# Performance work log

Measured on AMD Instinct MI355X. Metric: run time of the kernel, lower is better.

## Reference

```python
import jax, jax.numpy as jnp
import numpy as np

DIM = 768
NUM_HEADS = 12
HEAD_DIM = DIM // NUM_HEADS  # 64
IMG_W = 32
IMG_H = 32
B = 16
N = IMG_W * IMG_H + 1  # 1025 (CLS + grid)


def setup_inputs() -> dict:
    key = jax.random.key(0)
    k1, k2, k3, k4, k5 = jax.random.split(key, 5)
    x = jax.random.normal(k1, (B, N, DIM), dtype=jnp.float32)
    W_qkv = jax.random.normal(k2, (3 * DIM, DIM), dtype=jnp.float32) * 0.02
    W_proj = jax.random.normal(k3, (DIM, DIM), dtype=jnp.float32) * 0.02
    b_proj = jax.random.normal(k4, (DIM,), dtype=jnp.float32) * 0.02
    # learned mixed-RoPE frequencies, shape (2, num_heads * head_dim//2)
    freqs = jax.random.normal(k5, (2, NUM_HEADS * (HEAD_DIM // 2)), dtype=jnp.float32) * 0.1
    return {"x": x, "W_qkv": W_qkv, "W_proj": W_proj, "b_proj": b_proj, "freqs": freqs}


def _mixed_angles(freqs):
    # t_x = t % W, t_y = t // W over the flattened grid (init_t_xy)
    t = jnp.arange(IMG_W * IMG_H, dtype=jnp.float32)
    t_x = t % IMG_W
    t_y = jnp.floor(t / IMG_W)
    # outer products -> (N-1, H, hd/2) -> (H, N-1, hd/2); angle = fx + fy
    fx = (t_x[:, None] * freqs[0][None, :]).reshape(-1, NUM_HEADS, HEAD_DIM // 2)
    fy = (t_y[:, None] * freqs[1][None, :]).reshape(-1, NUM_HEADS, HEAD_DIM // 2)
    return (fx + fy).transpose(1, 0, 2)  # (H, N-1, hd/2)


def _apply_rope(t, cos, sin):
    # t: (B, H, N-1, hd); complex multiply on (even, odd) pairs
    pairs = t.reshape(*t.shape[:-1], HEAD_DIM // 2, 2)
    x0, x1 = pairs[..., 0], pairs[..., 1]
    o0 = x0 * cos - x1 * sin
    o1 = x0 * sin + x1 * cos
    return jnp.stack([o0, o1], axis=-1).reshape(t.shape)


def reference(x, W_qkv, W_proj, b_proj, freqs):
    Bx, Nx, C = x.shape
    scale = HEAD_DIM ** -0.5
    qkv = jnp.einsum('bnc,dc->bnd', x, W_qkv)  # Linear, no bias
    qkv = qkv.reshape(Bx, Nx, 3, NUM_HEADS, HEAD_DIM).transpose(2, 0, 3, 1, 4)
    q, k, v = qkv[0], qkv[1], qkv[2]  # (B, H, N, hd)

    ang = _mixed_angles(freqs)  # (H, N-1, hd/2)
    cos, sin = jnp.cos(ang), jnp.sin(ang)  # broadcast over batch

    # rotate all tokens except the leading CLS token
    q = jnp.concatenate([q[:, :, :1], _apply_rope(q[:, :, 1:], cos, sin)], axis=2)
    k = jnp.concatenate([k[:, :, :1], _apply_rope(k[:, :, 1:], cos, sin)], axis=2)

    attn = jax.nn.softmax(jnp.einsum('bhqd,bhkd->bhqk', q * scale, k), axis=-1)
    out = jnp.einsum('bhqk,bhkd->bhqd', attn, v)  # (B, H, N, hd)
    out = out.transpose(0, 2, 1, 3).reshape(Bx, Nx, C)
    return out @ W_proj.T + b_proj
```

## Files before the change

kernel.cpp:

```cpp
#include <hip/hip_runtime.h>
#include <math.h>

#define DIM     768
#define NH      12
#define HD      64
#define NTOK    1025
#define BATCH   16
#define MTOT    (BATCH * NTOK)
#define QKVD    (3 * DIM)

typedef short  short8  __attribute__((ext_vector_type(8)));
typedef short  short4v __attribute__((ext_vector_type(4)));
typedef float  f32x4   __attribute__((ext_vector_type(4)));

typedef const __attribute__((address_space(1))) void gvoid_t;
typedef __attribute__((address_space(3)))       void lvoid_t;
typedef __attribute__((address_space(3)))       char lchar_t;
#define GLD16(gsrc, ldst) __builtin_amdgcn_global_load_lds( \
    (gvoid_t*)(gsrc), (lvoid_t*)(ldst), 16, 0, 0)

static __device__ __forceinline__ unsigned int f2bf(float f) {
    unsigned int u = __float_as_uint(f);
    u += 0x7FFFu + ((u >> 16) & 1u);
    return u >> 16;
}

__device__ __forceinline__ void cvt8(const float* __restrict__ src,
                                     unsigned short* __restrict__ dst, int i) {
    float4 a = *(const float4*)(src + (size_t)i*8);
    float4 b = *(const float4*)(src + (size_t)i*8 + 4);
    uint4 pk;
    pk.x = f2bf(a.x) | (f2bf(a.y) << 16);
    pk.y = f2bf(a.z) | (f2bf(a.w) << 16);
    pk.z = f2bf(b.x) | (f2bf(b.y) << 16);
    pk.w = f2bf(b.z) | (f2bf(b.w) << 16);
    *(uint4*)(dst + (size_t)i*8) = pk;
}

__global__ __launch_bounds__(256) void cvt_bf16_kernel(
    const float* __restrict__ x, const float* __restrict__ Wq,
    const float* __restrict__ Wp,
    unsigned short* __restrict__ xb, unsigned short* __restrict__ Wqb,
    unsigned short* __restrict__ Wpb)
{
    const int stride = gridDim.x * blockDim.x;
    const int tid = blockIdx.x * blockDim.x + threadIdx.x;
    for (int i = tid; i < MTOT*DIM/8;  i += stride) cvt8(x,  xb,  i);
    for (int i = tid; i < QKVD*DIM/8;  i += stride) cvt8(Wq, Wqb, i);
    for (int i = tid; i < DIM*DIM/8;   i += stride) cvt8(Wp, Wpb, i);
}

__global__ __launch_bounds__(256) void rope_tab_kernel(
    const float* __restrict__ freqs, float2* __restrict__ tab)
{
    const int gid = blockIdx.x * 256 + threadIdx.x;
    const int p  = gid & 31;
    const int n1 = (gid >> 5) & 1023;
    const int h  = gid >> 15;
    const float tx = (float)(n1 & 31), ty = (float)(n1 >> 5);
    const float ang = tx * freqs[h*32 + p] + ty * freqs[384 + h*32 + p];
    float s, c;
    sincosf(ang, &s, &c);
    tab[gid] = make_float2(c, s);
}

__device__ __forceinline__ void gemm_core(
    const unsigned short* __restrict__ Wb,
    const unsigned short* __restrict__ Xb,
    int D0, int T0, int maxXrow,
    short* Ws, short* Xs, f32x4 acc[4][4], int tid)
{
    const int lane = tid & 63;
    const int wu   = __builtin_amdgcn_readfirstlane(tid >> 6);
    const int wr   = wu >> 1, wc = wu & 1;
    const int l4   = lane >> 4, l15 = lane & 15;

    const int srow = lane >> 3;
    const int schk = (lane & 7) ^ srow;
    const unsigned short* wsrc[4];
    const unsigned short* xsrc[4];
#pragma unroll
    for (int i = 0; i < 4; ++i) {
        int r = wu*32 + i*8 + srow;
        wsrc[i] = Wb + (size_t)(D0 + r) * DIM + schk*8;
        int xr = T0 + r; if (xr > maxXrow) xr = maxXrow;
        xsrc[i] = Xb + (size_t)xr * DIM + schk*8;
    }

    for (int kt = 0; kt < DIM/64; ++kt) {
        __syncthreads();
#pragma unroll
        for (int i = 0; i < 4; ++i) {
            GLD16(wsrc[i] + kt*64, &Ws[(wu*4 + i) * 512]);
            GLD16(xsrc[i] + kt*64, &Xs[(wu*4 + i) * 512]);
        }
        __syncthreads();

        short8 wf[4][2], xf[4][2];
#pragma unroll
        for (int f = 0; f < 4; ++f) {
            const int rw = wr*64 + f*16 + l15;
            const int rx = wc*64 + f*16 + l15;
#pragma unroll
            for (int kf = 0; kf < 2; ++kf) {
                wf[f][kf] = *(const short8*)&Ws[rw*64 + (((kf*4 + l4) ^ (rw & 7)) << 3)];
                xf[f][kf] = *(const short8*)&Xs[rx*64 + (((kf*4 + l4) ^ (rx & 7)) << 3)];
            }
        }
        __builtin_amdgcn_s_setprio(1);
#pragma unroll
        for (int kf = 0; kf < 2; ++kf)
#pragma unroll
            for (int fm = 0; fm < 4; ++fm)
#pragma unroll
                for (int fn = 0; fn < 4; ++fn)
                    acc[fm][fn] = __builtin_amdgcn_mfma_f32_16x16x32_bf16(
                        wf[fm][kf], xf[fn][kf], acc[fm][fn], 0, 0, 0);
        __builtin_amdgcn_s_setprio(0);
    }
}

__global__ __launch_bounds__(256) void qkv_gemm_kernel(
    const unsigned short* __restrict__ Wqb, const unsigned short* __restrict__ xb,
    const float2* __restrict__ tab,
    unsigned short* __restrict__ Qb, unsigned short* __restrict__ Kb,
    unsigned short* __restrict__ Vb)
{
    __shared__ __align__(16) short Ws[128*64];
    __shared__ __align__(16) short Xs[128*64];
    f32x4 acc[4][4] = {};
    const int tid = threadIdx.x;

    const int dd0 = blockIdx.x;
    int xc, j;
    if (dd0 >= 2304) { xc = 0; j = 288 + (dd0 - 2304); }
    else             { xc = dd0 & 7; j = dd0 >> 3; }
    const int D0 = (j % 18) * 128;
    const int T0 = (xc + 8 * (j / 18)) * 128;

    gemm_core(Wqb, xb, D0, T0, MTOT - 1, Ws, Xs, acc, tid);

    const int lane = tid & 63;
    const int wu = tid >> 6, wr = wu >> 1, wc = wu & 1;
    const int l4 = lane >> 4, l15 = lane & 15;
    const int which = D0 / DIM;
    unsigned short* dst = (which == 0) ? Qb : (which == 1) ? Kb : Vb;
    const float qs = (which == 0) ? 0.125f * 1.44269504089f : 1.f;

    unsigned bArr[4], nArr[4];
    bool vArr[4];
#pragma unroll
    for (int fn = 0; fn < 4; ++fn) {
        unsigned m = T0 + wc*64 + fn*16 + l15;
        vArr[fn] = m < MTOT;
        bArr[fn] = m / NTOK;
        nArr[fn] = m - bArr[fn]*NTOK;
    }
#pragma unroll
    for (int fm = 0; fm < 4; ++fm) {
        const int hcol = (D0 % DIM) + wr*64 + fm*16 + l4*4;
        const int h = hcol >> 6, dd = hcol & 63;
        const int p0 = dd >> 1;
#pragma unroll
        for (int fn = 0; fn < 4; ++fn) {
            if (!vArr[fn]) continue;
            f32x4 a = acc[fm][fn];
            const int n = nArr[fn];
            if (which < 2) {
                int n1 = n > 0 ? n - 1 : 0;
                float4 cs = *(const float4*)&tab[(size_t)(h*1024 + n1)*32 + p0];
                if (n == 0) cs = make_float4(1.f, 0.f, 1.f, 0.f);
                float e0 = a[0], od0 = a[1], e1 = a[2], od1 = a[3];
                a[0] = e0*cs.x - od0*cs.y;  a[1] = e0*cs.y + od0*cs.x;
                a[2] = e1*cs.z - od1*cs.w;  a[3] = e1*cs.w + od1*cs.z;
            }
            uint2 pk;
            pk.x = f2bf(a[0]*qs) | (f2bf(a[1]*qs) << 16);
            pk.y = f2bf(a[2]*qs) | (f2bf(a[3]*qs) << 16);
            *(uint2*)&dst[((size_t)(bArr[fn]*NH + h)*NTOK + n)*HD + dd] = pk;
        }
    }
}

__global__ __launch_bounds__(256) void attn_mfma_kernel(
    const unsigned short* __restrict__ Qb,
    const unsigned short* __restrict__ Kb,
    const unsigned short* __restrict__ Vb,
    unsigned short* __restrict__ Obf)
{
    __shared__ __align__(16) char KsR[2][8192];
    __shared__ __align__(16) char VtR[2][8192];
    __shared__ __align__(16) char PsR[4][4096];

    const int tid  = threadIdx.x;
    const int lane = tid & 63;
    const int w    = __builtin_amdgcn_readfirstlane(tid >> 6);
    const int l4   = lane >> 4, l15 = lane & 15, l7 = lane & 7;

    const int d    = blockIdx.x;
    const int xcd  = d & 7;
    const int s    = d >> 3;
    const int bh   = xcd * 24 + s / 9;
    const int q0   = (s % 9) * 128;
    const size_t base = (size_t)bh * NTOK * HD;

    short8 qf[2][2];
#pragma unroll
    for (int qg = 0; qg < 2; ++qg) {
        int qr = q0 + w*32 + qg*16 + l15;
        int qrc = qr < NTOK ? qr : NTOK - 1;
        qf[qg][0] = *(const short8*)(Qb + base + (size_t)qrc*HD + l4*8);
        qf[qg][1] = *(const short8*)(Qb + base + (size_t)qrc*HD + 32 + l4*8);
    }

    const short ONE = (short)0x3F80;
    const short8 ones = {ONE, ONE, ONE, ONE, ONE, ONE, ONE, ONE};

    f32x4 oA[4] = {}, oB[4] = {};
    f32x4 laccA = {}, laccB = {};

    const int ktokb = tid >> 3;
    const int kchk  = tid & 7;
    const int c0 = tid, c1 = tid + 256;
    const int vt0 = ((c0 >> 5) << 2) | ((c0 >> 1) & 3);
    const int vt1 = ((c1 >> 5) << 2) | ((c1 >> 1) & 3);
    const int vo0 = (((c0 >> 3) & 3) << 4) | ((c0 & 1) << 3);
    const int vo1 = (((c1 >> 3) & 3) << 4) | ((c1 & 1) << 3);
    char* Pw = &PsR[w][0];

#pragma unroll
    for (int i = 0; i < 2; ++i) {
        int tok = ktokb + i*32;
        int sc = kchk ^ (tok & 7);
        GLD16(Kb + base + (size_t)tok*HD + sc*8, &KsR[0][w*1024 + i*4096]);
    }
    GLD16(Vb + base + (size_t)vt0*HD + vo0, &VtR[0][w*1024]);
    GLD16(Vb + base + (size_t)vt1*HD + vo1, &VtR[0][4096 + w*1024]);

    for (int kt = 0; kt < 17; ++kt) {
        const int buf = kt & 1;
        __syncthreads();

        if (kt < 16) {
            const int nb = buf ^ 1;
#pragma unroll
            for (int i = 0; i < 2; ++i) {
                int tok = ktokb + i*32;
                int gk = (kt+1)*64 + tok; if (gk > NTOK-1) gk = NTOK-1;
                int sc = kchk ^ (tok & 7);
                GLD16(Kb + base + (size_t)gk*HD + sc*8, &KsR[nb][w*1024 + i*4096]);
            }
            int g0 = (kt+1)*64 + vt0; if (g0 > NTOK-1) g0 = NTOK-1;
            int g1 = (kt+1)*64 + vt1; if (g1 > NTOK-1) g1 = NTOK-1;
            GLD16(Vb + base + (size_t)g0*HD + vo0, &VtR[nb][w*1024]);
            GLD16(Vb + base + (size_t)g1*HD + vo1, &VtR[nb][4096 + w*1024]);
        }

        f32x4 sA[4] = {}, sB[4] = {};
        __builtin_amdgcn_s_setprio(1);
#pragma unroll
        for (int tg = 0; tg < 4; ++tg) {
            const int row = tg*16 + l15;
            short8 ka0 = *(const short8*)(&KsR[buf][0] + row*128 + ((l4 ^ l7) << 4));
            short8 ka1 = *(const short8*)(&KsR[buf][0] + row*128 + (((4 + l4) ^ l7) << 4));
            sA[tg] = __builtin_amdgcn_mfma_f32_16x16x32_bf16(ka0, qf[0][0], sA[tg], 0,0,0);
            sA[tg] = __builtin_amdgcn_mfma_f32_16x16x32_bf16(ka1, qf[0][1], sA[tg], 0,0,0);
            sB[tg] = __builtin_amdgcn_mfma_f32_16x16x32_bf16(ka0, qf[1][0], sB[tg], 0,0,0);
            sB[tg] = __builtin_amdgcn_mfma_f32_16x16x32_bf16(ka1, qf[1][1], sB[tg], 0,0,0);
        }
        __builtin_amdgcn_s_setprio(0);

        float pA[16], pB[16];
        if (kt == 16) {
#pragma unroll
            for (int tg = 0; tg < 4; ++tg)
#pragma unroll
                for (int r = 0; r < 4; ++r) {
                    int tok = 1024 + tg*16 + l4*4 + r;
                    float sa = (tok > 1024) ? -3e38f : sA[tg][r];
                    float sb = (tok > 1024) ? -3e38f : sB[tg][r];
                    pA[tg*4+r] = __builtin_exp2f(sa);
                    pB[tg*4+r] = __builtin_exp2f(sb);
                }
        } else {
#pragma unroll
            for (int tg = 0; tg < 4; ++tg)
#pragma unroll
                for (int r = 0; r < 4; ++r) {
                    pA[tg*4+r] = __builtin_exp2f(sA[tg][r]);
                    pB[tg*4+r] = __builtin_exp2f(sB[tg][r]);
                }
        }

#pragma unroll
        for (int tg = 0; tg < 4; ++tg) {
            unsigned k0a, k1a, k0b, k1b;
            asm volatile("v_cvt_pk_bf16_f32 %0, %1, %2" : "=v"(k0a) : "v"(pA[tg*4+0]), "v"(pA[tg*4+1]));
            asm volatile("v_cvt_pk_bf16_f32 %0, %1, %2" : "=v"(k1a) : "v"(pA[tg*4+2]), "v"(pA[tg*4+3]));
            asm volatile("v_cvt_pk_bf16_f32 %0, %1, %2" : "=v"(k0b) : "v"(pB[tg*4+0]), "v"(pB[tg*4+1]));
            asm volatile("v_cvt_pk_bf16_f32 %0, %1, %2" : "=v"(k1b) : "v"(pB[tg*4+2]), "v"(pB[tg*4+3]));
            const int chk = (((tg*2 + (l4 >> 1)) ^ l7) << 4) + (l4 & 1)*8;
            *(uint2*)(Pw + l15*128      + chk) = make_uint2(k0a, k1a);
            *(uint2*)(Pw + (16+l15)*128 + chk) = make_uint2(k0b, k1b);
        }
        __builtin_amdgcn_wave_barrier();

        const short8 pf00 = *(const short8*)(Pw + l15*128      + ((l4 ^ l7) << 4));
        const short8 pf01 = *(const short8*)(Pw + l15*128      + (((4+l4) ^ l7) << 4));
        const short8 pf10 = *(const short8*)(Pw + (16+l15)*128 + ((l4 ^ l7) << 4));
        const short8 pf11 = *(const short8*)(Pw + (16+l15)*128 + (((4+l4) ^ l7) << 4));

        __builtin_amdgcn_s_setprio(1);
        laccA = __builtin_amdgcn_mfma_f32_16x16x32_bf16(ones, pf00, laccA, 0,0,0);
        laccA = __builtin_amdgcn_mfma_f32_16x16x32_bf16(ones, pf01, laccA, 0,0,0);
        laccB = __builtin_amdgcn_mfma_f32_16x16x32_bf16(ones, pf10, laccB, 0,0,0);
        laccB = __builtin_amdgcn_mfma_f32_16x16x32_bf16(ones, pf11, laccB, 0,0,0);
        __builtin_amdgcn_s_setprio(0);

        const unsigned trb = (unsigned)(unsigned long long)
            (lchar_t*)(&VtR[buf][0] + (l4 << 10) + (l15 << 3));
        short4v r0a, r0b, r1a, r1b, r2a, r2b, r3a, r3b;

        asm volatile(
            "ds_read_b64_tr_b16 %0, %8 offset:0\n\t"
            "ds_read_b64_tr_b16 %1, %8 offset:512\n\t"
            "ds_read_b64_tr_b16 %2, %8 offset:128\n\t"
            "ds_read_b64_tr_b16 %3, %8 offset:640\n\t"
            "ds_read_b64_tr_b16 %4, %8 offset:256\n\t"
            "ds_read_b64_tr_b16 %5, %8 offset:768\n\t"
            "ds_read_b64_tr_b16 %6, %8 offset:384\n\t"
            "ds_read_b64_tr_b16 %7, %8 offset:896\n\t"
            "s_waitcnt lgkmcnt(0)"
            : "=&v"(r0a), "=&v"(r0b), "=&v"(r1a), "=&v"(r1b),
              "=&v"(r2a), "=&v"(r2b), "=&v"(r3a), "=&v"(r3b)
            : "v"(trb) : "memory");
        __builtin_amdgcn_sched_barrier(0);
        {
            short8 v0 = __builtin_shufflevector(r0a, r0b, 0,1,2,3,4,5,6,7);
            short8 v1 = __builtin_shufflevector(r1a, r1b, 0,1,2,3,4,5,6,7);
            short8 v2 = __builtin_shufflevector(r2a, r2b, 0,1,2,3,4,5,6,7);
            short8 v3 = __builtin_shufflevector(r3a, r3b, 0,1,2,3,4,5,6,7);
            __builtin_amdgcn_s_setprio(1);
            oA[0] = __builtin_amdgcn_mfma_f32_16x16x32_bf16(v0, pf00, oA[0], 0,0,0);
            oB[0] = __builtin_amdgcn_mfma_f32_16x16x32_bf16(v0, pf10, oB[0], 0,0,0);
            oA[1] = __builtin_amdgcn_mfma_f32_16x16x32_bf16(v1, pf00, oA[1], 0,0,0);
            oB[1] = __builtin_amdgcn_mfma_f32_16x16x32_bf16(v1, pf10, oB[1], 0,0,0);
            oA[2] = __builtin_amdgcn_mfma_f32_16x16x32_bf16(v2, pf00, oA[2], 0,0,0);
            oB[2] = __builtin_amdgcn_mfma_f32_16x16x32_bf16(v2, pf10, oB[2], 0,0,0);
            oA[3] = __builtin_amdgcn_mfma_f32_16x16x32_bf16(v3, pf00, oA[3], 0,0,0);
            oB[3] = __builtin_amdgcn_mfma_f32_16x16x32_bf16(v3, pf10, oB[3], 0,0,0);
            __builtin_amdgcn_s_setprio(0);
        }
        asm volatile(
            "ds_read_b64_tr_b16 %0, %8 offset:4096\n\t"
            "ds_read_b64_tr_b16 %1, %8 offset:4608\n\t"
            "ds_read_b64_tr_b16 %2, %8 offset:4224\n\t"
            "ds_read_b64_tr_b16 %3, %8 offset:4736\n\t"
            "ds_read_b64_tr_b16 %4, %8 offset:4352\n\t"
            "ds_read_b64_tr_b16 %5, %8 offset:4864\n\t"
            "ds_read_b64_tr_b16 %6, %8 offset:4480\n\t"
            "ds_read_b64_tr_b16 %7, %8 offset:4992\n\t"
            "s_waitcnt lgkmcnt(0)"
            : "=&v"(r0a), "=&v"(r0b), "=&v"(r1a), "=&v"(r1b),
              "=&v"(r2a), "=&v"(r2b), "=&v"(r3a), "=&v"(r3b)
            : "v"(trb) : "memory");
        __builtin_amdgcn_sched_barrier(0);
        {
            short8 v0 = __builtin_shufflevector(r0a, r0b, 0,1,2,3,4,5,6,7);
            short8 v1 = __builtin_shufflevector(r1a, r1b, 0,1,2,3,4,5,6,7);
            short8 v2 = __builtin_shufflevector(r2a, r2b, 0,1,2,3,4,5,6,7);
            short8 v3 = __builtin_shufflevector(r3a, r3b, 0,1,2,3,4,5,6,7);
            __builtin_amdgcn_s_setprio(1);
            oA[0] = __builtin_amdgcn_mfma_f32_16x16x32_bf16(v0, pf01, oA[0], 0,0,0);
            oB[0] = __builtin_amdgcn_mfma_f32_16x16x32_bf16(v0, pf11, oB[0], 0,0,0);
            oA[1] = __builtin_amdgcn_mfma_f32_16x16x32_bf16(v1, pf01, oA[1], 0,0,0);
            oB[1] = __builtin_amdgcn_mfma_f32_16x16x32_bf16(v1, pf11, oB[1], 0,0,0);
            oA[2] = __builtin_amdgcn_mfma_f32_16x16x32_bf16(v2, pf01, oA[2], 0,0,0);
            oB[2] = __builtin_amdgcn_mfma_f32_16x16x32_bf16(v2, pf11, oB[2], 0,0,0);
            oA[3] = __builtin_amdgcn_mfma_f32_16x16x32_bf16(v3, pf01, oA[3], 0,0,0);
            oB[3] = __builtin_amdgcn_mfma_f32_16x16x32_bf16(v3, pf11, oB[3], 0,0,0);
            __builtin_amdgcn_s_setprio(0);
        }
    }

    const float liA = 1.f / laccA[0];
    const float liB = 1.f / laccB[0];
    const int b = bh / NH, h = bh % NH;
    const int qA = q0 + w*32 + l15;
    const int qB = qA + 16;
    if (qA < NTOK) {
        unsigned short* p = Obf + ((size_t)b*NTOK + qA)*DIM + h*HD + l4*4;
#pragma unroll
        for (int dg = 0; dg < 4; ++dg) {
            uint2 pk;
            pk.x = f2bf(oA[dg][0]*liA) | (f2bf(oA[dg][1]*liA) << 16);
            pk.y = f2bf(oA[dg][2]*liA) | (f2bf(oA[dg][3]*liA) << 16);
            *(uint2*)(p + dg*16) = pk;
        }
    }
    if (qB < NTOK) {
        unsigned short* p = Obf + ((size_t)b*NTOK + qB)*DIM + h*HD + l4*4;
#pragma unroll
        for (int dg = 0; dg < 4; ++dg) {
            uint2 pk;
            pk.x = f2bf(oB[dg][0]*liB) | (f2bf(oB[dg][1]*liB) << 16);
            pk.y = f2bf(oB[dg][2]*liB) | (f2bf(oB[dg][3]*liB) << 16);
            *(uint2*)(p + dg*16) = pk;
        }
    }
}

__global__ __launch_bounds__(256) void proj_gemm_kernel(
    const unsigned short* __restrict__ Wpb, const unsigned short* __restrict__ Obf,
    const float* __restrict__ bp, float* __restrict__ out)
{
    __shared__ __align__(16) short Ws[128*64];
    __shared__ __align__(16) short Xs[128*64];
    f32x4 acc[4][4] = {};
    const int tid = threadIdx.x;

    const int dd0 = blockIdx.x;
    int xc, j;
    if (dd0 >= 768) { xc = 0; j = 96 + (dd0 - 768); }
    else            { xc = dd0 & 7; j = dd0 >> 3; }
    const int D0 = (j % 6) * 128;
    const int T0 = (xc + 8 * (j / 6)) * 128;

    gemm_core(Wpb, Obf, D0, T0, MTOT - 1, Ws, Xs, acc, tid);

    const int lane = tid & 63;
    const int wu = tid >> 6, wr = wu >> 1, wc = wu & 1;
    const int l4 = lane >> 4, l15 = lane & 15;

    unsigned mArr[4];
    bool vArr[4];
#pragma unroll
    for (int fn = 0; fn < 4; ++fn) {
        unsigned m = T0 + wc*64 + fn*16 + l15;
        mArr[fn] = m;
        vArr[fn] = m < MTOT;
    }
#pragma unroll
    for (int fm = 0; fm < 4; ++fm) {
        const int nG = D0 + wr*64 + fm*16 + l4*4;
        const float4 bias = *(const float4*)&bp[nG];
#pragma unroll
        for (int fn = 0; fn < 4; ++fn) {
            if (!vArr[fn]) continue;
            f32x4 a = acc[fm][fn];
            float4 v = make_float4(a[0]+bias.x, a[1]+bias.y, a[2]+bias.z, a[3]+bias.w);
            *(float4*)&out[(size_t)mArr[fn]*DIM + nG] = v;
        }
    }
}

extern "C" void kernel_launch(void* const* d_in, const int* in_sizes, int n_in,
                              void* d_out, int out_size, void* d_ws, size_t ws_size,
                              hipStream_t stream)
{
    const float* x     = (const float*)d_in[0];
    const float* Wqkv  = (const float*)d_in[1];
    const float* Wp    = (const float*)d_in[2];
    const float* bp    = (const float*)d_in[3];
    const float* freqs = (const float*)d_in[4];
    float* out = (float*)d_out;

    const size_t SZ = (size_t)BATCH * NH * NTOK * HD;
    unsigned short* Qb  = (unsigned short*)d_ws;
    unsigned short* Kb  = Qb + SZ;
    unsigned short* Vb  = Kb + SZ;
    unsigned short* Obf = Vb + SZ;
    unsigned short* xb  = Obf + SZ;
    unsigned short* Wqb = xb + SZ;
    unsigned short* Wpb = Wqb + (size_t)QKVD * DIM;
    float2*         tab = (float2*)(Wpb + (size_t)DIM * DIM);

    cvt_bf16_kernel<<<2048, 256, 0, stream>>>(x, Wqkv, Wp, xb, Wqb, Wpb);
    rope_tab_kernel<<<1536, 256, 0, stream>>>(freqs, tab);
    qkv_gemm_kernel<<<2322, 256, 0, stream>>>(Wqb, xb, tab, Qb, Kb, Vb);
    attn_mfma_kernel<<<1728, 256, 0, stream>>>(Qb, Kb, Vb, Obf);
    proj_gemm_kernel<<<774, 256, 0, stream>>>(Wpb, Obf, bp, out);
}
```

Measured before the change: 263.1 us.

## Switch attention to 32x32x16 MFMA with register-resident P via permlane swaps

The attention kernel moves from 16x16x32 to 32x32x16 bf16 MFMA tiles, with each wave owning 32 query rows as the B operand. The softmax probabilities are converted to bf16 and rearranged in registers with v_permlane32_swap, which removes the per-wave LDS staging buffer, its wave barrier and the reads back. The row sum is now accumulated in scalar float adds plus one cross-half shuffle instead of extra ones-vector MFMAs. The intent is to cut LDS traffic and MFMA issue count, at the cost of larger accumulator register use and trickier lane mappings.

```diff
diff --git a/kernel.cpp b/kernel.cpp
--- a/kernel.cpp
+++ b/kernel.cpp
@@ -12,6 +12,7 @@
 typedef short  short8  __attribute__((ext_vector_type(8)));
 typedef short  short4v __attribute__((ext_vector_type(4)));
 typedef float  f32x4   __attribute__((ext_vector_type(4)));
+typedef float  f32x16  __attribute__((ext_vector_type(16)));
 
 typedef const __attribute__((address_space(1))) void gvoid_t;
 typedef __attribute__((address_space(3)))       void lvoid_t;
@@ -190,34 +191,31 @@
 {
     __shared__ __align__(16) char KsR[2][8192];
     __shared__ __align__(16) char VtR[2][8192];
-    __shared__ __align__(16) char PsR[4][4096];
 
     const int tid  = threadIdx.x;
     const int lane = tid & 63;
     const int w    = __builtin_amdgcn_readfirstlane(tid >> 6);
-    const int l4   = lane >> 4, l15 = lane & 15, l7 = lane & 7;
-
-    const int d    = blockIdx.x;
-    const int xcd  = d & 7;
-    const int s    = d >> 3;
+    const int l31  = lane & 31;
+    const int hh   = lane >> 5;
+
+    const int bid  = blockIdx.x;
+    const int xcd  = bid & 7;
+    const int s    = bid >> 3;
     const int bh   = xcd * 24 + s / 9;
     const int q0   = (s % 9) * 128;
     const size_t base = (size_t)bh * NTOK * HD;
 
-    short8 qf[2][2];
-#pragma unroll
-    for (int qg = 0; qg < 2; ++qg) {
-        int qr = q0 + w*32 + qg*16 + l15;
-        int qrc = qr < NTOK ? qr : NTOK - 1;
-        qf[qg][0] = *(const short8*)(Qb + base + (size_t)qrc*HD + l4*8);
-        qf[qg][1] = *(const short8*)(Qb + base + (size_t)qrc*HD + 32 + l4*8);
-    }
-
-    const short ONE = (short)0x3F80;
-    const short8 ones = {ONE, ONE, ONE, ONE, ONE, ONE, ONE, ONE};
-
-    f32x4 oA[4] = {}, oB[4] = {};
-    f32x4 laccA = {}, laccB = {};
+    const int q  = q0 + w*32 + l31;
+    const int qc = q < NTOK ? q : NTOK - 1;
+    const unsigned short* qp = Qb + base + (size_t)qc*HD + hh*8;
+    const short8 qf0 = *(const short8*)(qp);
+    const short8 qf1 = *(const short8*)(qp + 16);
+    const short8 qf2 = *(const short8*)(qp + 32);
+    const short8 qf3 = *(const short8*)(qp + 48);
+
+    f32x16 o0 = {0,0,0,0,0,0,0,0,0,0,0,0,0,0,0,0};
+    f32x16 o1 = o0;
+    float lsum = 0.f;
 
     const int ktokb = tid >> 3;
     const int kchk  = tid & 7;
@@ -226,7 +224,9 @@
     const int vt1 = ((c1 >> 5) << 2) | ((c1 >> 1) & 3);
     const int vo0 = (((c0 >> 3) & 3) << 4) | ((c0 & 1) << 3);
     const int vo1 = (((c1 >> 3) & 3) << 4) | ((c1 & 1) << 3);
-    char* Pw = &PsR[w][0];
+
+    const unsigned trlane = (unsigned)((hh << 10) | (((lane >> 4) & 1) << 7)
+                                       | ((lane & 15) << 3));
 
 #pragma unroll
     for (int i = 0; i < 2; ++i) {
@@ -256,156 +256,93 @@
             GLD16(Vb + base + (size_t)g1*HD + vo1, &VtR[nb][4096 + w*1024]);
         }
 
-        f32x4 sA[4] = {}, sB[4] = {};
+        const char* Kc = &KsR[buf][0];
+        f32x16 s0 = {0,0,0,0,0,0,0,0,0,0,0,0,0,0,0,0};
+        f32x16 s1 = s0;
         __builtin_amdgcn_s_setprio(1);
 #pragma unroll
-        for (int tg = 0; tg < 4; ++tg) {
-            const int row = tg*16 + l15;
-            short8 ka0 = *(const short8*)(&KsR[buf][0] + row*128 + ((l4 ^ l7) << 4));
-            short8 ka1 = *(const short8*)(&KsR[buf][0] + row*128 + (((4 + l4) ^ l7) << 4));
-            sA[tg] = __builtin_amdgcn_mfma_f32_16x16x32_bf16(ka0, qf[0][0], sA[tg], 0,0,0);
-            sA[tg] = __builtin_amdgcn_mfma_f32_16x16x32_bf16(ka1, qf[0][1], sA[tg], 0,0,0);
-            sB[tg] = __builtin_amdgcn_mfma_f32_16x16x32_bf16(ka0, qf[1][0], sB[tg], 0,0,0);
-            sB[tg] = __builtin_amdgcn_mfma_f32_16x16x32_bf16(ka1, qf[1][1], sB[tg], 0,0,0);
+        for (int g = 0; g < 4; ++g) {
+            const int a = l31*128 + ((((g << 1) | hh) ^ (l31 & 7)) << 4);
+            short8 ka0 = *(const short8*)(Kc + a);
+            short8 ka1 = *(const short8*)(Kc + a + 4096);
+            const short8 qg = (g == 0) ? qf0 : (g == 1) ? qf1 : (g == 2) ? qf2 : qf3;
+            s0 = __builtin_amdgcn_mfma_f32_32x32x16_bf16(ka0, qg, s0, 0, 0, 0);
+            s1 = __builtin_amdgcn_mfma_f32_32x32x16_bf16(ka1, qg, s1, 0, 0, 0);
         }
         __builtin_amdgcn_s_setprio(0);
 
-        float pA[16], pB[16];
         if (kt == 16) {
 #pragma unroll
-            for (int tg = 0; tg < 4; ++tg)
-#pragma unroll
-                for (int r = 0; r < 4; ++r) {
-                    int tok = 1024 + tg*16 + l4*4 + r;
-                    float sa = (tok > 1024) ? -3e38f : sA[tg][r];
-                    float sb = (tok > 1024) ? -3e38f : sB[tg][r];
-                    pA[tg*4+r] = __builtin_exp2f(sa);
-                    pB[tg*4+r] = __builtin_exp2f(sb);
-                }
-        } else {
-#pragma unroll
-            for (int tg = 0; tg < 4; ++tg)
-#pragma unroll
-                for (int r = 0; r < 4; ++r) {
-                    pA[tg*4+r] = __builtin_exp2f(sA[tg][r]);
-                    pB[tg*4+r] = __builtin_exp2f(sB[tg][r]);
-                }
-        }
-
-#pragma unroll
-        for (int tg = 0; tg < 4; ++tg) {
-            unsigned k0a, k1a, k0b, k1b;
-            asm volatile("v_cvt_pk_bf16_f32 %0, %1, %2" : "=v"(k0a) : "v"(pA[tg*4+0]), "v"(pA[tg*4+1]));
-            asm volatile("v_cvt_pk_bf16_f32 %0, %1, %2" : "=v"(k1a) : "v"(pA[tg*4+2]), "v"(pA[tg*4+3]));
-            asm volatile("v_cvt_pk_bf16_f32 %0, %1, %2" : "=v"(k0b) : "v"(pB[tg*4+0]), "v"(pB[tg*4+1]));
-            asm volatile("v_cvt_pk_bf16_f32 %0, %1, %2" : "=v"(k1b) : "v"(pB[tg*4+2]), "v"(pB[tg*4+3]));
-            const int chk = (((tg*2 + (l4 >> 1)) ^ l7) << 4) + (l4 & 1)*8;
-            *(uint2*)(Pw + l15*128      + chk) = make_uint2(k0a, k1a);
-            *(uint2*)(Pw + (16+l15)*128 + chk) = make_uint2(k0b, k1b);
-        }
-        __builtin_amdgcn_wave_barrier();
-
-        const short8 pf00 = *(const short8*)(Pw + l15*128      + ((l4 ^ l7) << 4));
-        const short8 pf01 = *(const short8*)(Pw + l15*128      + (((4+l4) ^ l7) << 4));
-        const short8 pf10 = *(const short8*)(Pw + (16+l15)*128 + ((l4 ^ l7) << 4));
-        const short8 pf11 = *(const short8*)(Pw + (16+l15)*128 + (((4+l4) ^ l7) << 4));
-
-        __builtin_amdgcn_s_setprio(1);
-        laccA = __builtin_amdgcn_mfma_f32_16x16x32_bf16(ones, pf00, laccA, 0,0,0);
-        laccA = __builtin_amdgcn_mfma_f32_16x16x32_bf16(ones, pf01, laccA, 0,0,0);
-        laccB = __builtin_amdgcn_mfma_f32_16x16x32_bf16(ones, pf10, laccB, 0,0,0);
-        laccB = __builtin_amdgcn_mfma_f32_16x16x32_bf16(ones, pf11, laccB, 0,0,0);
-        __builtin_amdgcn_s_setprio(0);
+            for (int r = 1; r < 16; ++r) s0[r] = -3e38f;
+#pragma unroll
+            for (int r = 0; r < 16; ++r) s1[r] = -3e38f;
+            if (lane >= 32) s0[0] = -3e38f;
+        }
+
+        short8 pb0, pb1, pb2, pb3;
+#define EXP_PB(S, PB_LO, PB_HI) { \
+        unsigned cp_[8]; \
+        _Pragma("unroll") \
+        for (int j_ = 0; j_ < 8; ++j_) { \
+            float ea_ = __builtin_exp2f(S[2*j_]); \
+            float eb_ = __builtin_exp2f(S[2*j_+1]); \
+            lsum += ea_ + eb_; \
+            asm("v_cvt_pk_bf16_f32 %0, %1, %2" : "=v"(cp_[j_]) : "v"(ea_), "v"(eb_)); \
+        } \
+        asm volatile("v_permlane32_swap_b32 %0, %1" : "+v"(cp_[0]), "+v"(cp_[2])); \
+        asm volatile("v_permlane32_swap_b32 %0, %1" : "+v"(cp_[1]), "+v"(cp_[3])); \
+        asm volatile("v_permlane32_swap_b32 %0, %1" : "+v"(cp_[4]), "+v"(cp_[6])); \
+        asm volatile("v_permlane32_swap_b32 %0, %1" : "+v"(cp_[5]), "+v"(cp_[7])); \
+        union { unsigned u[4]; short8 s8; } tl_, th_; \
+        tl_.u[0] = cp_[0]; tl_.u[1] = cp_[1]; tl_.u[2] = cp_[2]; tl_.u[3] = cp_[3]; \
+        th_.u[0] = cp_[4]; th_.u[1] = cp_[5]; th_.u[2] = cp_[6]; th_.u[3] = cp_[7]; \
+        PB_LO = tl_.s8; PB_HI = th_.s8; }
+
+        EXP_PB(s0, pb0, pb1);
+        EXP_PB(s1, pb2, pb3);
+#undef EXP_PB
 
         const unsigned trb = (unsigned)(unsigned long long)
-            (lchar_t*)(&VtR[buf][0] + (l4 << 10) + (l15 << 3));
-        short4v r0a, r0b, r1a, r1b, r2a, r2b, r3a, r3b;
-
-        asm volatile(
-            "ds_read_b64_tr_b16 %0, %8 offset:0\n\t"
-            "ds_read_b64_tr_b16 %1, %8 offset:512\n\t"
-            "ds_read_b64_tr_b16 %2, %8 offset:128\n\t"
-            "ds_read_b64_tr_b16 %3, %8 offset:640\n\t"
-            "ds_read_b64_tr_b16 %4, %8 offset:256\n\t"
-            "ds_read_b64_tr_b16 %5, %8 offset:768\n\t"
-            "ds_read_b64_tr_b16 %6, %8 offset:384\n\t"
-            "ds_read_b64_tr_b16 %7, %8 offset:896\n\t"
-            "s_waitcnt lgkmcnt(0)"
-            : "=&v"(r0a), "=&v"(r0b), "=&v"(r1a), "=&v"(r1b),
-              "=&v"(r2a), "=&v"(r2b), "=&v"(r3a), "=&v"(r3b)
-            : "v"(trb) : "memory");
-        __builtin_amdgcn_sched_barrier(0);
-        {
-            short8 v0 = __builtin_shufflevector(r0a, r0b, 0,1,2,3,4,5,6,7);
-            short8 v1 = __builtin_shufflevector(r1a, r1b, 0,1,2,3,4,5,6,7);
-            short8 v2 = __builtin_shufflevector(r2a, r2b, 0,1,2,3,4,5,6,7);
-            short8 v3 = __builtin_shufflevector(r3a, r3b, 0,1,2,3,4,5,6,7);
-            __builtin_amdgcn_s_setprio(1);
-            oA[0] = __builtin_amdgcn_mfma_f32_16x16x32_bf16(v0, pf00, oA[0], 0,0,0);
-            oB[0] = __builtin_amdgcn_mfma_f32_16x16x32_bf16(v0, pf10, oB[0], 0,0,0);
-            oA[1] = __builtin_amdgcn_mfma_f32_16x16x32_bf16(v1, pf00, oA[1], 0,0,0);
-            oB[1] = __builtin_amdgcn_mfma_f32_16x16x32_bf16(v1, pf10, oB[1], 0,0,0);
-            oA[2] = __builtin_amdgcn_mfma_f32_16x16x32_bf16(v2, pf00, oA[2], 0,0,0);
-            oB[2] = __builtin_amdgcn_mfma_f32_16x16x32_bf16(v2, pf10, oB[2], 0,0,0);
-            oA[3] = __builtin_amdgcn_mfma_f32_16x16x32_bf16(v3, pf00, oA[3], 0,0,0);
-            oB[3] = __builtin_amdgcn_mfma_f32_16x16x32_bf16(v3, pf10, oB[3], 0,0,0);
-            __builtin_amdgcn_s_setprio(0);
-        }
-        asm volatile(
-            "ds_read_b64_tr_b16 %0, %8 offset:4096\n\t"
-            "ds_read_b64_tr_b16 %1, %8 offset:4608\n\t"
-            "ds_read_b64_tr_b16 %2, %8 offset:4224\n\t"
-            "ds_read_b64_tr_b16 %3, %8 offset:4736\n\t"
-            "ds_read_b64_tr_b16 %4, %8 offset:4352\n\t"
-            "ds_read_b64_tr_b16 %5, %8 offset:4864\n\t"
-            "ds_read_b64_tr_b16 %6, %8 offset:4480\n\t"
-            "ds_read_b64_tr_b16 %7, %8 offset:4992\n\t"
-            "s_waitcnt lgkmcnt(0)"
-            : "=&v"(r0a), "=&v"(r0b), "=&v"(r1a), "=&v"(r1b),
-              "=&v"(r2a), "=&v"(r2b), "=&v"(r3a), "=&v"(r3b)
-            : "v"(trb) : "memory");
-        __builtin_amdgcn_sched_barrier(0);
-        {
-            short8 v0 = __builtin_shufflevector(r0a, r0b, 0,1,2,3,4,5,6,7);
-            short8 v1 = __builtin_shufflevector(r1a, r1b, 0,1,2,3,4,5,6,7);
-            short8 v2 = __builtin_shufflevector(r2a, r2b, 0,1,2,3,4,5,6,7);
-            short8 v3 = __builtin_shufflevector(r3a, r3b, 0,1,2,3,4,5,6,7);
-            __builtin_amdgcn_s_setprio(1);
-            oA[0] = __builtin_amdgcn_mfma_f32_16x16x32_bf16(v0, pf01, oA[0], 0,0,0);
-            oB[0] = __builtin_amdgcn_mfma_f32_16x16x32_bf16(v0, pf11, oB[0], 0,0,0);
-            oA[1] = __builtin_amdgcn_mfma_f32_16x16x32_bf16(v1, pf01, oA[1], 0,0,0);
-            oB[1] = __builtin_amdgcn_mfma_f32_16x16x32_bf16(v1, pf11, oB[1], 0,0,0);
-            oA[2] = __builtin_amdgcn_mfma_f32_16x16x32_bf16(v2, pf01, oA[2], 0,0,0);
-            oB[2] = __builtin_amdgcn_mfma_f32_16x16x32_bf16(v2, pf11, oB[2], 0,0,0);
-            oA[3] = __builtin_amdgcn_mfma_f32_16x16x32_bf16(v3, pf01, oA[3], 0,0,0);
-            oB[3] = __builtin_amdgcn_mfma_f32_16x16x32_bf16(v3, pf11, oB[3], 0,0,0);
-            __builtin_amdgcn_s_setprio(0);
-        }
-    }
-
-    const float liA = 1.f / laccA[0];
-    const float liB = 1.f / laccB[0];
-    const int b = bh / NH, h = bh % NH;
-    const int qA = q0 + w*32 + l15;
-    const int qB = qA + 16;
-    if (qA < NTOK) {
-        unsigned short* p = Obf + ((size_t)b*NTOK + qA)*DIM + h*HD + l4*4;
-#pragma unroll
-        for (int dg = 0; dg < 4; ++dg) {
-            uint2 pk;
-            pk.x = f2bf(oA[dg][0]*liA) | (f2bf(oA[dg][1]*liA) << 16);
-            pk.y = f2bf(oA[dg][2]*liA) | (f2bf(oA[dg][3]*liA) << 16);
-            *(uint2*)(p + dg*16) = pk;
-        }
-    }
-    if (qB < NTOK) {
-        unsigned short* p = Obf + ((size_t)b*NTOK + qB)*DIM + h*HD + l4*4;
-#pragma unroll
-        for (int dg = 0; dg < 4; ++dg) {
-            uint2 pk;
-            pk.x = f2bf(oB[dg][0]*liB) | (f2bf(oB[dg][1]*liB) << 16);
-            pk.y = f2bf(oB[dg][2]*liB) | (f2bf(oB[dg][3]*liB) << 16);
-            *(uint2*)(p + dg*16) = pk;
+            (lchar_t*)(&VtR[buf][0]) + trlane;
+        short4v r0a, r0b, r1a, r1b;
+#define PV_KG(O0, O1, O2, O3, PB) { \
+        asm volatile( \
+            "ds_read_b64_tr_b16 %0, %4 offset:" #O0 "\n\t" \
+            "ds_read_b64_tr_b16 %1, %4 offset:" #O1 "\n\t" \
+            "ds_read_b64_tr_b16 %2, %4 offset:" #O2 "\n\t" \
+            "ds_read_b64_tr_b16 %3, %4 offset:" #O3 "\n\t" \
+            "s_waitcnt lgkmcnt(0)" \
+            : "=&v"(r0a), "=&v"(r0b), "=&v"(r1a), "=&v"(r1b) \
+            : "v"(trb) : "memory"); \
+        __builtin_amdgcn_sched_barrier(0); \
+        { short8 v0_ = __builtin_shufflevector(r0a, r0b, 0,1,2,3,4,5,6,7); \
+          short8 v1_ = __builtin_shufflevector(r1a, r1b, 0,1,2,3,4,5,6,7); \
+          __builtin_amdgcn_s_setprio(1); \
+          o0 = __builtin_amdgcn_mfma_f32_32x32x16_bf16(v0_, PB, o0, 0, 0, 0); \
+          o1 = __builtin_amdgcn_mfma_f32_32x32x16_bf16(v1_, PB, o1, 0, 0, 0); \
+          __builtin_amdgcn_s_setprio(0); } }
+
+        PV_KG(0,    512,  256,  768,  pb0)
+        PV_KG(2048, 2560, 2304, 2816, pb1)
+        PV_KG(4096, 4608, 4352, 4864, pb2)
+        PV_KG(6144, 6656, 6400, 6912, pb3)
+#undef PV_KG
+    }
+
+    lsum += __shfl_xor(lsum, 32);
+    const float li = 1.f / lsum;
+    const int bb = bh / NH, hd = bh % NH;
+    if (q < NTOK) {
+        unsigned short* p = Obf + ((size_t)bb*NTOK + q)*DIM + hd*HD;
+#pragma unroll
+        for (int m = 0; m < 4; ++m) {
+            uint2 k0, k1;
+            k0.x = f2bf(o0[4*m+0]*li) | (f2bf(o0[4*m+1]*li) << 16);
+            k0.y = f2bf(o0[4*m+2]*li) | (f2bf(o0[4*m+3]*li) << 16);
+            *(uint2*)(p + 8*m + 4*hh) = k0;
+            k1.x = f2bf(o1[4*m+0]*li) | (f2bf(o1[4*m+1]*li) << 16);
+            k1.y = f2bf(o1[4*m+2]*li) | (f2bf(o1[4*m+3]*li) << 16);
+            *(uint2*)(p + 32 + 8*m + 4*hh) = k1;
         }
     }
 }
```

Result: slower. 274.5 us (+4.3%).
